# Optimization experiments

Measured on AMD Instinct MI355X. Metric: run time of the kernel, lower is better.

## Reference

```python
import jax, jax.numpy as jnp
import numpy as np

N_EMBD = 2048
N_Q = 32
N_KV = 8
GROUP = N_Q // N_KV   # 4
HD = N_EMBD // N_Q    # 64
BASE = 10000.0
NEG_INF = -1e30


def _rope(x):
    """Rotate-half RoPE on last dim; positions 1..t along dim -2 (as in the
    original _build_cache which uses arange(1, seq_len+1))."""
    t, d = x.shape[-2], x.shape[-1]
    d2 = d // 2
    theta = 1.0 / (BASE ** (jnp.arange(0, d, 2, dtype=jnp.float32) / d))  # (d/2,)
    pos = jnp.arange(1, t + 1, dtype=jnp.float32)                          # (t,)
    ang = pos[:, None] * theta[None, :]                                    # (t, d/2)
    ang = jnp.concatenate([ang, ang], axis=-1)                             # (t, d)
    sin, cos = jnp.sin(ang), jnp.cos(ang)
    rot = jnp.concatenate([-x[..., d2:], x[..., :d2]], axis=-1)
    return x * cos + rot * sin


def setup_inputs() -> dict:
    key = jax.random.key(0)
    ks = jax.random.split(key, 5)
    b, t = 2, 1024
    s = 1.0 / np.sqrt(N_EMBD)
    return {
        "x": jax.random.normal(ks[0], (b, t, N_EMBD), dtype=jnp.float32),
        "wq": jax.random.normal(ks[1], (N_EMBD, N_EMBD), dtype=jnp.float32) * s,
        "bq": jnp.zeros((N_EMBD,), dtype=jnp.float32),
        "wk": jax.random.normal(ks[2], (N_EMBD, N_KV * HD), dtype=jnp.float32) * s,
        "bk": jnp.zeros((N_KV * HD,), dtype=jnp.float32),
        "wv": jax.random.normal(ks[3], (N_EMBD, N_KV * HD), dtype=jnp.float32) * s,
        "bv": jnp.zeros((N_KV * HD,), dtype=jnp.float32),
        "wo": jax.random.normal(ks[4], (N_EMBD, N_EMBD), dtype=jnp.float32) * s,
        "bo": jnp.zeros((N_EMBD,), dtype=jnp.float32),
    }


def reference(x, wq, bq, wk, bk, wv, bv, wo, bo):
    b, t, _ = x.shape
    q = x @ wq + bq                                   # (b, t, E)
    k = x @ wk + bk                                   # (b, t, NKV*HD)
    v = x @ wv + bv
    q = q.reshape(b, t, N_Q, HD).transpose(0, 2, 1, 3)        # (b, nq, t, d)
    q = q.reshape(b, N_KV, GROUP, t, HD)                      # (b, hkv, g, t, d)
    k = k.reshape(b, t, N_KV, HD).transpose(0, 2, 1, 3)       # (b, hkv, t, d)
    v = v.reshape(b, t, N_KV, HD).transpose(0, 2, 1, 3)
    q = _rope(q)
    k = _rope(k)
    scale = jnp.sqrt(jnp.float32(HD))
    att = jnp.einsum("bhgqd,bhkd->bhgqk", q, k) / scale       # (b, hkv, g, t, t)
    causal = jnp.tril(jnp.ones((t, t), dtype=bool))
    att = jnp.where(causal, att, NEG_INF)
    att = jax.nn.softmax(att, axis=-1)
    out = jnp.einsum("bhgqk,bhkd->bhgqd", att, v)             # (b, hkv, g, t, d)
    out = out.transpose(0, 3, 1, 2, 4).reshape(b, t, N_EMBD)  # (b, t, E)
    return out @ wo + bo
```

## Files before the change

kernel.cpp:

```cpp
#include <hip/hip_runtime.h>
#include <hip/hip_bf16.h>
#include <cstdint>


typedef __attribute__((ext_vector_type(8))) short short8;
typedef __attribute__((ext_vector_type(4))) short short4v;
typedef __attribute__((ext_vector_type(4))) float f32x4;

__device__ inline short f2b(float f) {
  union { float f; unsigned u; } v; v.f = f;
  unsigned r = v.u + 0x7fffu + ((v.u >> 16) & 1u);
  return (short)(r >> 16);
}

__device__ inline float exp2_fast(float x) {
  float r;
  asm("v_exp_f32 %0, %1" : "=v"(r) : "v"(x));
  return r;
}

__device__ inline void gl_lds16(const void* g, void* l) {
  __builtin_amdgcn_global_load_lds((const __attribute__((address_space(1))) void*)g,
                                   (__attribute__((address_space(3))) void*)l,
                                   16, 0, 0);
}

__global__ void cast_x_kernel(const float* __restrict__ x, short* __restrict__ xb, int n4) {
  int i = blockIdx.x * 256 + threadIdx.x;
  if (i >= n4) return;
  float4 v = ((const float4*)x)[i];
  short4v o; o.x = f2b(v.x); o.y = f2b(v.y); o.z = f2b(v.z); o.w = f2b(v.w);
  ((short4v*)xb)[i] = o;
}

__global__ void wtrans_all(const float* __restrict__ wq, const float* __restrict__ wk,
                           const float* __restrict__ wv, const float* __restrict__ wo,
                           short* __restrict__ WqkvT, short* __restrict__ woT) {
  __shared__ float tile[64][65];
  const int bx = blockIdx.x;
  const float* W; short* WT; int N, off, nb;
  if (bx < 32)      { W = wq; WT = WqkvT; N = 2048; off = 0;    nb = bx * 64; }
  else if (bx < 40) { W = wk; WT = WqkvT; N = 512;  off = 2048; nb = (bx - 32) * 64; }
  else if (bx < 48) { W = wv; WT = WqkvT; N = 512;  off = 2560; nb = (bx - 40) * 64; }
  else              { W = wo; WT = woT;   N = 2048; off = 0;    nb = (bx - 48) * 64; }
  const int kb = blockIdx.y * 64;
  const int tid = threadIdx.x;
  const int c = tid & 63, r0 = tid >> 6;
#pragma unroll
  for (int s = 0; s < 16; ++s) {
    int k = r0 + s * 4;
    tile[c][k] = W[(size_t)(kb + k) * N + nb + c];
  }
  __syncthreads();
#pragma unroll
  for (int s = 0; s < 16; ++s) {
    int n = r0 + s * 4;
    WT[(size_t)(off + nb + n) * 2048 + kb + c] = f2b(tile[n][c]);
  }
}

__device__ __forceinline__ void gemm_loop_bk64(const short* __restrict__ Ag,
                                               const short* __restrict__ Bg,
                                               short* lA, short* lB,
                                               int w, int l15, int q4,
                                               f32x4 acc[2][4]) {
  const int K = 2048, NS = 32;
  const int q4x = q4 ^ ((l15 >> 1) & 3);
  auto stage = [&](int s, int d) {
    const short* As = Ag + s * 64;
    const short* Bs = Bg + s * 64;
    short* a = lA + d * 8192 + w * 512;
    gl_lds16(As, a);
    gl_lds16(As + 64 * K, a + 2048);
    gl_lds16(As + 32, a + 4096);
    gl_lds16(As + 64 * K + 32, a + 6144);
    short* bp = lB + d * 4096 + w * 512;
    gl_lds16(Bs, bp);
    gl_lds16(Bs + 32, bp + 2048);
  };
  stage(0, 0);
  for (int s = 0; s < NS; ++s) {
    const int d = s & 1;
    __syncthreads();
    if (s + 1 < NS) stage(s + 1, d ^ 1);
#pragma unroll
    for (int ks = 0; ks < 2; ++ks) {
      const short* ap = lA + d * 8192 + ks * 4096;
      const short* bp = lB + d * 4096 + ks * 2048;
      short8 af[2], bf[4];
#pragma unroll
      for (int mf = 0; mf < 2; ++mf) af[mf] = *(const short8*)(ap + (w * 32 + mf * 16 + l15) * 32 + q4x * 8);
#pragma unroll
      for (int nf = 0; nf < 4; ++nf) bf[nf] = *(const short8*)(bp + (nf * 16 + l15) * 32 + q4x * 8);
#pragma unroll
      for (int mf = 0; mf < 2; ++mf)
#pragma unroll
        for (int nf = 0; nf < 4; ++nf)
          acc[mf][nf] = __builtin_amdgcn_mfma_f32_16x16x32_bf16(af[mf], bf[nf], acc[mf][nf], 0, 0, 0);
    }
  }
}

__launch_bounds__(256, 3)
__global__ void gemm_qkv(const short* __restrict__ A, const short* __restrict__ BT,
                         const float* __restrict__ bq, const float* __restrict__ bk,
                         const float* __restrict__ bv,
                         short* __restrict__ Qb, short* __restrict__ Kb,
                         short* __restrict__ VTb) {
  __shared__ __align__(16) short lA[16384];
  __shared__ __align__(16) short lB[8192];
  const int K = 2048;
  const int tid = threadIdx.x, lane = tid & 63, w = tid >> 6;
  const int q4 = lane >> 4, l15 = lane & 15;
  const int bn = blockIdx.x * 64, bm = blockIdx.y * 128;

  const int swzc = ((tid & 3) ^ ((tid >> 3) & 3)) << 3;
  const short* Ag = A + (size_t)(bm + (tid >> 2)) * K + swzc;
  const short* Bg = BT + (size_t)(bn + (tid >> 2)) * K + swzc;

  f32x4 acc[2][4];
  const f32x4 fz = {0.f, 0.f, 0.f, 0.f};
#pragma unroll
  for (int i = 0; i < 2; ++i)
#pragma unroll
    for (int j = 0; j < 4; ++j) acc[i][j] = fz;

  gemm_loop_bk64(Ag, Bg, lA, lB, w, l15, q4, acc);

  const float L2T = 0.4152410118609203f;
  const float theta_a = exp2_fast(-(float)l15 * L2T);
  const float theta_b = exp2_fast(-(float)(l15 + 16) * L2T);
  const float s2 = 0.18033688011112042f;

  if (bn < 2048) {
    const int h = bn >> 6;
    float bb0 = bq[bn + l15], bb1 = bq[bn + 16 + l15], bb2 = bq[bn + 32 + l15], bb3 = bq[bn + 48 + l15];
#pragma unroll
    for (int mf = 0; mf < 2; ++mf)
#pragma unroll
      for (int r = 0; r < 4; ++r) {
        int row = bm + w * 32 + mf * 16 + q4 * 4 + r;
        int batch = row >> 10, t = row & 1023;
        float pos = (float)(t + 1);
        float sa, ca, sb, cb;
        __sincosf(pos * theta_a, &sa, &ca);
        __sincosf(pos * theta_b, &sb, &cb);
        float x0 = acc[mf][0][r] + bb0, x2 = acc[mf][2][r] + bb2;
        float x1 = acc[mf][1][r] + bb1, x3 = acc[mf][3][r] + bb3;
        size_t base = ((size_t)(batch * 32 + h) * 1024 + t) * 64;
        Qb[base + l15]      = f2b((x0 * ca - x2 * sa) * s2);
        Qb[base + l15 + 32] = f2b((x2 * ca + x0 * sa) * s2);
        Qb[base + l15 + 16] = f2b((x1 * cb - x3 * sb) * s2);
        Qb[base + l15 + 48] = f2b((x3 * cb + x1 * sb) * s2);
      }
  } else if (bn < 2560) {
    const int co = bn - 2048;
    const int hkv = co >> 6;
    float bb0 = bk[co + l15], bb1 = bk[co + 16 + l15], bb2 = bk[co + 32 + l15], bb3 = bk[co + 48 + l15];
#pragma unroll
    for (int mf = 0; mf < 2; ++mf)
#pragma unroll
      for (int r = 0; r < 4; ++r) {
        int row = bm + w * 32 + mf * 16 + q4 * 4 + r;
        int batch = row >> 10, t = row & 1023;
        float pos = (float)(t + 1);
        float sa, ca, sb, cb;
        __sincosf(pos * theta_a, &sa, &ca);
        __sincosf(pos * theta_b, &sb, &cb);
        float x0 = acc[mf][0][r] + bb0, x2 = acc[mf][2][r] + bb2;
        float x1 = acc[mf][1][r] + bb1, x3 = acc[mf][3][r] + bb3;
        size_t base = (size_t)(batch * 8 + hkv) * 65536 + t * 32;
        Kb[base + l15]              = f2b(x0 * ca - x2 * sa);
        Kb[base + l15 + 16]         = f2b(x1 * cb - x3 * sb);
        Kb[base + 32768 + l15]      = f2b(x2 * ca + x0 * sa);
        Kb[base + 32768 + l15 + 16] = f2b(x3 * cb + x1 * sb);
      }
  } else {
    const int co = bn - 2560;
    const int hkv = co >> 6;
    float bb[4];
#pragma unroll
    for (int nf = 0; nf < 4; ++nf) bb[nf] = bv[co + nf * 16 + l15];
    const int batch = (bm + w * 32) >> 10;
    const size_t vbase = (size_t)(batch * 8 + hkv) * 65536;
#pragma unroll
    for (int mf = 0; mf < 2; ++mf) {
      const int t0 = (bm + w * 32 + mf * 16 + q4 * 4) & 1023;
      const size_t rbase = vbase + (size_t)(t0 >> 5) * 2048 + (t0 & 31);
#pragma unroll
      for (int nf = 0; nf < 4; ++nf) {
        short4v pk;
#pragma unroll
        for (int r = 0; r < 4; ++r) pk[r] = f2b(acc[mf][nf][r] + bb[nf]);
        *(short4v*)(VTb + rbase + (nf * 16 + l15) * 32) = pk;
      }
    }
  }
}

#define PROW 72
__launch_bounds__(256, 3)
__global__ void attn5_kernel(const short* __restrict__ Qb, const short* __restrict__ Kb,
                             const short* __restrict__ VTb, short* __restrict__ AO) {
  __shared__ __align__(16) short lK[2][128 * 32];
  __shared__ __align__(16) short lVT[4][64 * 32];
  __shared__ __align__(16) short lP[4][2][16 * PROW];
  const int tid = threadIdx.x, lane = tid & 63, w = tid >> 6;
  const int q4 = lane >> 4, l15 = lane & 15;
  const int q4x = q4 ^ ((l15 >> 1) & 3);
  const int swzc = ((tid & 3) ^ ((tid >> 3) & 3)) << 3;
  const int qt = (int)gridDim.x - 1 - (int)blockIdx.x;
  const int h = blockIdx.y, b = blockIdx.z;
  const int hkv = h >> 2;
  const int qb = qt * 128 + w * 32;
  const int kdiag = qb >> 6;
  const int ns = qt + 1;

  const short* Qg = Qb + (size_t)(b * 32 + h) * 65536;
  const short* Kg = Kb + (size_t)(b * 8 + hkv) * 65536;
  const short* Vg = VTb + (size_t)(b * 8 + hkv) * 65536;

  short8 qf[2][2];
#pragma unroll
  for (int mf = 0; mf < 2; ++mf) {
    const short* qr = Qg + (size_t)(qb + mf * 16 + l15) * 64 + q4 * 8;
    qf[mf][0] = *(const short8*)(qr);
    qf[mf][1] = *(const short8*)(qr + 32);
  }

  const f32x4 fz = {0.f, 0.f, 0.f, 0.f};
  f32x4 o[2][4], ol[2];
#pragma unroll
  for (int mf = 0; mf < 2; ++mf) {
    ol[mf] = fz;
#pragma unroll
    for (int i = 0; i < 4; ++i) o[mf][i] = fz;
  }
  short8 ones;
#pragma unroll
  for (int i = 0; i < 8; ++i) ones[i] = (short)0x3F80;

  for (int s = 0; s < ns; ++s) {
    {
      const short* Ksrc = Kg + (size_t)(s * 128 + (tid >> 2)) * 32 + swzc;
      short* ldst = (short*)lK + w * 512;
      gl_lds16(Ksrc, ldst);
      gl_lds16(Ksrc + 64 * 32, ldst + 2048);
      gl_lds16(Ksrc + 32768, ldst + 4096);
      gl_lds16(Ksrc + 32768 + 64 * 32, ldst + 6144);
      const short* Vsrc = Vg + (size_t)(s * 4) * 2048 + (tid >> 2) * 32 + swzc;
      short* vdst = (short*)lVT + w * 512;
#pragma unroll
      for (int c = 0; c < 4; ++c) gl_lds16(Vsrc + c * 2048, vdst + c * 2048);
    }
    __syncthreads();

#pragma unroll
    for (int ki = 0; ki < 2; ++ki) {
      const int ktg = s * 2 + ki;
      if (ktg <= kdiag) {
        short8 kf0[4], kf1[4];
#pragma unroll
        for (int nt = 0; nt < 4; ++nt) {
          kf0[nt] = *(const short8*)((short*)lK + (ki * 64 + nt * 16 + l15) * 32 + q4x * 8);
          kf1[nt] = *(const short8*)((short*)lK + 4096 + (ki * 64 + nt * 16 + l15) * 32 + q4x * 8);
        }
        const bool diag = (ktg == kdiag);
#pragma unroll
        for (int mf = 0; mf < 2; ++mf) {
          f32x4 sv[4];
#pragma unroll
          for (int nt = 0; nt < 4; ++nt) {
            f32x4 z = __builtin_amdgcn_mfma_f32_16x16x32_bf16(qf[mf][0], kf0[nt], fz, 0, 0, 0);
            sv[nt] = __builtin_amdgcn_mfma_f32_16x16x32_bf16(qf[mf][1], kf1[nt], z, 0, 0, 0);
          }
          if (diag) {
#pragma unroll
            for (int r = 0; r < 4; ++r) {
              const int qrow = qb + mf * 16 + q4 * 4 + r;
              const int col = ktg * 64 + l15;
#pragma unroll
              for (int nt = 0; nt < 4; ++nt)
                if (col + nt * 16 > qrow) sv[nt][r] = -1e30f;
            }
          }
          short* lPm = lP[w][mf];
#pragma unroll
          for (int r = 0; r < 4; ++r)
#pragma unroll
            for (int nt = 0; nt < 4; ++nt)
              lPm[(q4 * 4 + r) * PROW + nt * 16 + l15] = f2b(exp2_fast(sv[nt][r] - 16.f));
        }

        short8 vf0[4], vf1[4];
#pragma unroll
        for (int dt = 0; dt < 4; ++dt) {
          vf0[dt] = *(const short8*)((short*)lVT + (2 * ki) * 2048 + (dt * 16 + l15) * 32 + q4x * 8);
          vf1[dt] = *(const short8*)((short*)lVT + (2 * ki + 1) * 2048 + (dt * 16 + l15) * 32 + q4x * 8);
        }
#pragma unroll
        for (int mf = 0; mf < 2; ++mf) {
          const short* lPm = lP[w][mf];
          short8 pf0 = *(const short8*)(lPm + l15 * PROW + q4 * 8);
          short8 pf1 = *(const short8*)(lPm + l15 * PROW + 32 + q4 * 8);
          ol[mf] = __builtin_amdgcn_mfma_f32_16x16x32_bf16(pf0, ones, ol[mf], 0, 0, 0);
          ol[mf] = __builtin_amdgcn_mfma_f32_16x16x32_bf16(pf1, ones, ol[mf], 0, 0, 0);
#pragma unroll
          for (int dt = 0; dt < 4; ++dt) {
            o[mf][dt] = __builtin_amdgcn_mfma_f32_16x16x32_bf16(pf0, vf0[dt], o[mf][dt], 0, 0, 0);
            o[mf][dt] = __builtin_amdgcn_mfma_f32_16x16x32_bf16(pf1, vf1[dt], o[mf][dt], 0, 0, 0);
          }
        }
      }
    }
    __syncthreads();
  }

#pragma unroll
  for (int mf = 0; mf < 2; ++mf)
#pragma unroll
    for (int r = 0; r < 4; ++r) {
      float inv = __builtin_amdgcn_rcpf(ol[mf][r]);
      int row = qb + mf * 16 + q4 * 4 + r;
#pragma unroll
      for (int dt = 0; dt < 4; ++dt)
        AO[(size_t)(b * 1024 + row) * 2048 + h * 64 + dt * 16 + l15] = f2b(o[mf][dt][r] * inv);
    }
}

__launch_bounds__(256, 3)
__global__ void gemm_out(const short* __restrict__ A, const short* __restrict__ BT,
                         float* __restrict__ C, const float* __restrict__ bias,
                         int N, int K) {
  __shared__ __align__(16) short lA[16384];
  __shared__ __align__(16) short lB[8192];
  const int tid = threadIdx.x, lane = tid & 63, w = tid >> 6;
  const int q4 = lane >> 4, l15 = lane & 15;
  const int bn = blockIdx.x * 64, bm = blockIdx.y * 128;

  const int swzc = ((tid & 3) ^ ((tid >> 3) & 3)) << 3;
  const short* Ag = A + (size_t)(bm + (tid >> 2)) * K + swzc;
  const short* Bg = BT + (size_t)(bn + (tid >> 2)) * K + swzc;

  f32x4 acc[2][4];
  const f32x4 fz = {0.f, 0.f, 0.f, 0.f};
#pragma unroll
  for (int i = 0; i < 2; ++i)
#pragma unroll
    for (int j = 0; j < 4; ++j) acc[i][j] = fz;

  gemm_loop_bk64(Ag, Bg, lA, lB, w, l15, q4, acc);

#pragma unroll
  for (int mf = 0; mf < 2; ++mf)
#pragma unroll
    for (int nf = 0; nf < 4; ++nf) {
      int col = bn + nf * 16 + l15;
      float bb = bias[col];
#pragma unroll
      for (int r = 0; r < 4; ++r) {
        int row = bm + w * 32 + mf * 16 + q4 * 4 + r;
        C[(size_t)row * N + col] = acc[mf][nf][r] + bb;
      }
    }
}

extern "C" void kernel_launch(void* const* d_in, const int* in_sizes, int n_in,
                              void* d_out, int out_size, void* d_ws, size_t ws_size,
                              hipStream_t stream) {
  const float* x  = (const float*)d_in[0];
  const float* wq = (const float*)d_in[1];
  const float* bq = (const float*)d_in[2];
  const float* wk = (const float*)d_in[3];
  const float* bk = (const float*)d_in[4];
  const float* wv = (const float*)d_in[5];
  const float* bv = (const float*)d_in[6];
  const float* wo = (const float*)d_in[7];
  const float* bo = (const float*)d_in[8];
  float* out = (float*)d_out;
  const int B = in_sizes[0] / (1024 * 2048);
  const int M = B * 1024;

  char* ws = (char*)d_ws;
  size_t off = 0;
  auto alloc = [&](size_t bytes) -> char* {
    char* p = ws + off;
    off += (bytes + 255) & ~(size_t)255;
    return p;
  };
  short* xb    = (short*)alloc((size_t)M * 2048 * 2);
  short* WqkvT = (short*)alloc((size_t)3072 * 2048 * 2);
  short* woT   = (short*)alloc((size_t)2048 * 2048 * 2);
  short* Qb    = (short*)alloc((size_t)B * 32 * 1024 * 64 * 2);
  short* Kb    = (short*)alloc((size_t)B * 8 * 2 * 1024 * 32 * 2);
  short* VTb   = (short*)alloc((size_t)B * 8 * 32 * 64 * 32 * 2);
  short* AO    = (short*)alloc((size_t)M * 2048 * 2);

  cast_x_kernel<<<(M * 2048 / 4 + 255) / 256, 256, 0, stream>>>(x, xb, M * 2048 / 4);
  wtrans_all<<<dim3(80, 32), 256, 0, stream>>>(wq, wk, wv, wo, WqkvT, woT);
  gemm_qkv<<<dim3(48, M / 128), 256, 0, stream>>>(xb, WqkvT, bq, bk, bv, Qb, Kb, VTb);
  attn5_kernel<<<dim3(8, 32, B), 256, 0, stream>>>(Qb, Kb, VTb, AO);
  gemm_out<<<dim3(32, M / 128), 256, 0, stream>>>(AO, woT, out, bo, 2048, 2048);
}
```

Baseline: 206.2 us.

## Replace block-shared LDS K/V staging with single-wave blocks loading K/V directly

```diff
diff --git a/kernel.cpp b/kernel.cpp
--- a/kernel.cpp
+++ b/kernel.cpp
@@ -199,22 +199,17 @@
 }
 
 #define PROW 72
-__launch_bounds__(256, 3)
-__global__ void attn5_kernel(const short* __restrict__ Qb, const short* __restrict__ Kb,
+__launch_bounds__(64, 2)
+__global__ void attn6_kernel(const short* __restrict__ Qb, const short* __restrict__ Kb,
                              const short* __restrict__ VTb, short* __restrict__ AO) {
-  __shared__ __align__(16) short lK[2][128 * 32];
-  __shared__ __align__(16) short lVT[4][64 * 32];
-  __shared__ __align__(16) short lP[4][2][16 * PROW];
-  const int tid = threadIdx.x, lane = tid & 63, w = tid >> 6;
+  __shared__ __align__(16) short lP[2][16 * PROW];
+  const int lane = threadIdx.x;
   const int q4 = lane >> 4, l15 = lane & 15;
-  const int q4x = q4 ^ ((l15 >> 1) & 3);
-  const int swzc = ((tid & 3) ^ ((tid >> 3) & 3)) << 3;
-  const int qt = (int)gridDim.x - 1 - (int)blockIdx.x;
+  const int qt = 31 - (int)blockIdx.x;
   const int h = blockIdx.y, b = blockIdx.z;
   const int hkv = h >> 2;
-  const int qb = qt * 128 + w * 32;
+  const int qb = qt * 32;
   const int kdiag = qb >> 6;
-  const int ns = qt + 1;
 
   const short* Qg = Qb + (size_t)(b * 32 + h) * 65536;
   const short* Kg = Kb + (size_t)(b * 8 + hkv) * 65536;
@@ -240,80 +235,68 @@
 #pragma unroll
   for (int i = 0; i < 8; ++i) ones[i] = (short)0x3F80;
 
-  for (int s = 0; s < ns; ++s) {
-    {
-      const short* Ksrc = Kg + (size_t)(s * 128 + (tid >> 2)) * 32 + swzc;
-      short* ldst = (short*)lK + w * 512;
-      gl_lds16(Ksrc, ldst);
-      gl_lds16(Ksrc + 64 * 32, ldst + 2048);
-      gl_lds16(Ksrc + 32768, ldst + 4096);
-      gl_lds16(Ksrc + 32768 + 64 * 32, ldst + 6144);
-      const short* Vsrc = Vg + (size_t)(s * 4) * 2048 + (tid >> 2) * 32 + swzc;
-      short* vdst = (short*)lVT + w * 512;
-#pragma unroll
-      for (int c = 0; c < 4; ++c) gl_lds16(Vsrc + c * 2048, vdst + c * 2048);
-    }
-    __syncthreads();
-
-#pragma unroll
-    for (int ki = 0; ki < 2; ++ki) {
-      const int ktg = s * 2 + ki;
-      if (ktg <= kdiag) {
-        short8 kf0[4], kf1[4];
-#pragma unroll
-        for (int nt = 0; nt < 4; ++nt) {
-          kf0[nt] = *(const short8*)((short*)lK + (ki * 64 + nt * 16 + l15) * 32 + q4x * 8);
-          kf1[nt] = *(const short8*)((short*)lK + 4096 + (ki * 64 + nt * 16 + l15) * 32 + q4x * 8);
+  short8 kf0[4], kf1[4], vf0[4], vf1[4];
+  auto loadK = [&](int ktg) {
+    const short* kb0 = Kg + (size_t)(ktg * 64 + l15) * 32 + q4 * 8;
+#pragma unroll
+    for (int nt = 0; nt < 4; ++nt) kf0[nt] = *(const short8*)(kb0 + nt * 512);
+#pragma unroll
+    for (int nt = 0; nt < 4; ++nt) kf1[nt] = *(const short8*)(kb0 + 32768 + nt * 512);
+  };
+  auto loadV = [&](int ktg) {
+    const short* vb = Vg + (size_t)(2 * ktg) * 2048 + l15 * 32 + q4 * 8;
+#pragma unroll
+    for (int dt = 0; dt < 4; ++dt) vf0[dt] = *(const short8*)(vb + dt * 512);
+#pragma unroll
+    for (int dt = 0; dt < 4; ++dt) vf1[dt] = *(const short8*)(vb + 2048 + dt * 512);
+  };
+
+  loadK(0);
+  for (int ktg = 0; ktg <= kdiag; ++ktg) {
+    loadV(ktg);
+    f32x4 sv[2][4];
+#pragma unroll
+    for (int mf = 0; mf < 2; ++mf)
+#pragma unroll
+      for (int nt = 0; nt < 4; ++nt) {
+        f32x4 z = __builtin_amdgcn_mfma_f32_16x16x32_bf16(qf[mf][0], kf0[nt], fz, 0, 0, 0);
+        sv[mf][nt] = __builtin_amdgcn_mfma_f32_16x16x32_bf16(qf[mf][1], kf1[nt], z, 0, 0, 0);
+      }
+    if (ktg == kdiag) {
+#pragma unroll
+      for (int mf = 0; mf < 2; ++mf)
+#pragma unroll
+        for (int r = 0; r < 4; ++r) {
+          const int qrow = qb + mf * 16 + q4 * 4 + r;
+          const int col = ktg * 64 + l15;
+#pragma unroll
+          for (int nt = 0; nt < 4; ++nt)
+            if (col + nt * 16 > qrow) sv[mf][nt][r] = -1e30f;
         }
-        const bool diag = (ktg == kdiag);
-#pragma unroll
-        for (int mf = 0; mf < 2; ++mf) {
-          f32x4 sv[4];
-#pragma unroll
-          for (int nt = 0; nt < 4; ++nt) {
-            f32x4 z = __builtin_amdgcn_mfma_f32_16x16x32_bf16(qf[mf][0], kf0[nt], fz, 0, 0, 0);
-            sv[nt] = __builtin_amdgcn_mfma_f32_16x16x32_bf16(qf[mf][1], kf1[nt], z, 0, 0, 0);
-          }
-          if (diag) {
-#pragma unroll
-            for (int r = 0; r < 4; ++r) {
-              const int qrow = qb + mf * 16 + q4 * 4 + r;
-              const int col = ktg * 64 + l15;
-#pragma unroll
-              for (int nt = 0; nt < 4; ++nt)
-                if (col + nt * 16 > qrow) sv[nt][r] = -1e30f;
-            }
-          }
-          short* lPm = lP[w][mf];
-#pragma unroll
-          for (int r = 0; r < 4; ++r)
-#pragma unroll
-            for (int nt = 0; nt < 4; ++nt)
-              lPm[(q4 * 4 + r) * PROW + nt * 16 + l15] = f2b(exp2_fast(sv[nt][r] - 16.f));
-        }
-
-        short8 vf0[4], vf1[4];
-#pragma unroll
-        for (int dt = 0; dt < 4; ++dt) {
-          vf0[dt] = *(const short8*)((short*)lVT + (2 * ki) * 2048 + (dt * 16 + l15) * 32 + q4x * 8);
-          vf1[dt] = *(const short8*)((short*)lVT + (2 * ki + 1) * 2048 + (dt * 16 + l15) * 32 + q4x * 8);
-        }
-#pragma unroll
-        for (int mf = 0; mf < 2; ++mf) {
-          const short* lPm = lP[w][mf];
-          short8 pf0 = *(const short8*)(lPm + l15 * PROW + q4 * 8);
-          short8 pf1 = *(const short8*)(lPm + l15 * PROW + 32 + q4 * 8);
-          ol[mf] = __builtin_amdgcn_mfma_f32_16x16x32_bf16(pf0, ones, ol[mf], 0, 0, 0);
-          ol[mf] = __builtin_amdgcn_mfma_f32_16x16x32_bf16(pf1, ones, ol[mf], 0, 0, 0);
-#pragma unroll
-          for (int dt = 0; dt < 4; ++dt) {
-            o[mf][dt] = __builtin_amdgcn_mfma_f32_16x16x32_bf16(pf0, vf0[dt], o[mf][dt], 0, 0, 0);
-            o[mf][dt] = __builtin_amdgcn_mfma_f32_16x16x32_bf16(pf1, vf1[dt], o[mf][dt], 0, 0, 0);
-          }
-        }
-      }
-    }
-    __syncthreads();
+    }
+    if (ktg < kdiag) loadK(ktg + 1);
+#pragma unroll
+    for (int mf = 0; mf < 2; ++mf) {
+      short* lPm = lP[mf];
+#pragma unroll
+      for (int r = 0; r < 4; ++r)
+#pragma unroll
+        for (int nt = 0; nt < 4; ++nt)
+          lPm[(q4 * 4 + r) * PROW + nt * 16 + l15] = f2b(exp2_fast(sv[mf][nt][r] - 16.f));
+    }
+#pragma unroll
+    for (int mf = 0; mf < 2; ++mf) {
+      const short* lPm = lP[mf];
+      short8 pf0 = *(const short8*)(lPm + l15 * PROW + q4 * 8);
+      short8 pf1 = *(const short8*)(lPm + l15 * PROW + 32 + q4 * 8);
+      ol[mf] = __builtin_amdgcn_mfma_f32_16x16x32_bf16(pf0, ones, ol[mf], 0, 0, 0);
+      ol[mf] = __builtin_amdgcn_mfma_f32_16x16x32_bf16(pf1, ones, ol[mf], 0, 0, 0);
+#pragma unroll
+      for (int dt = 0; dt < 4; ++dt) {
+        o[mf][dt] = __builtin_amdgcn_mfma_f32_16x16x32_bf16(pf0, vf0[dt], o[mf][dt], 0, 0, 0);
+        o[mf][dt] = __builtin_amdgcn_mfma_f32_16x16x32_bf16(pf1, vf1[dt], o[mf][dt], 0, 0, 0);
+      }
+    }
   }
 
 #pragma unroll
@@ -399,6 +382,6 @@
   cast_x_kernel<<<(M * 2048 / 4 + 255) / 256, 256, 0, stream>>>(x, xb, M * 2048 / 4);
   wtrans_all<<<dim3(80, 32), 256, 0, stream>>>(wq, wk, wv, wo, WqkvT, woT);
   gemm_qkv<<<dim3(48, M / 128), 256, 0, stream>>>(xb, WqkvT, bq, bk, bv, Qb, Kb, VTb);
-  attn5_kernel<<<dim3(8, 32, B), 256, 0, stream>>>(Qb, Kb, VTb, AO);
+  attn6_kernel<<<dim3(32, 32, B), 64, 0, stream>>>(Qb, Kb, VTb, AO);
   gemm_out<<<dim3(32, M / 128), 256, 0, stream>>>(AO, woT, out, bo, 2048, 2048);
 }
```

Result: no change. 209.8 us (+1.8%).

## Double-buffer K/V tiles in attention with 64-key stages and prefetch

Applied to the files above, without the earlier changes.

```diff
diff --git a/kernel.cpp b/kernel.cpp
--- a/kernel.cpp
+++ b/kernel.cpp
@@ -200,10 +200,10 @@
 
 #define PROW 72
 __launch_bounds__(256, 3)
-__global__ void attn5_kernel(const short* __restrict__ Qb, const short* __restrict__ Kb,
+__global__ void attn8_kernel(const short* __restrict__ Qb, const short* __restrict__ Kb,
                              const short* __restrict__ VTb, short* __restrict__ AO) {
-  __shared__ __align__(16) short lK[2][128 * 32];
-  __shared__ __align__(16) short lVT[4][64 * 32];
+  __shared__ __align__(16) short lK[2][2 * 64 * 32];
+  __shared__ __align__(16) short lVT[2][2 * 64 * 32];
   __shared__ __align__(16) short lP[4][2][16 * PROW];
   const int tid = threadIdx.x, lane = tid & 63, w = tid >> 6;
   const int q4 = lane >> 4, l15 = lane & 15;
@@ -214,7 +214,7 @@
   const int hkv = h >> 2;
   const int qb = qt * 128 + w * 32;
   const int kdiag = qb >> 6;
-  const int ns = qt + 1;
+  const int ns = 2 * qt + 2;
 
   const short* Qg = Qb + (size_t)(b * 32 + h) * 65536;
   const short* Kg = Kb + (size_t)(b * 8 + hkv) * 65536;
@@ -240,80 +240,80 @@
 #pragma unroll
   for (int i = 0; i < 8; ++i) ones[i] = (short)0x3F80;
 
+  auto stage = [&](int s, int d) {
+    const short* Ksrc = Kg + (size_t)(s * 64 + (tid >> 2)) * 32 + swzc;
+    short* kd = (short*)lK + d * 4096 + w * 512;
+    gl_lds16(Ksrc, kd);
+    gl_lds16(Ksrc + 32768, kd + 2048);
+    const short* Vsrc = Vg + (size_t)(2 * s) * 2048 + (tid >> 2) * 32 + swzc;
+    short* vd = (short*)lVT + d * 4096 + w * 512;
+    gl_lds16(Vsrc, vd);
+    gl_lds16(Vsrc + 2048, vd + 2048);
+  };
+
+  stage(0, 0);
   for (int s = 0; s < ns; ++s) {
-    {
-      const short* Ksrc = Kg + (size_t)(s * 128 + (tid >> 2)) * 32 + swzc;
-      short* ldst = (short*)lK + w * 512;
-      gl_lds16(Ksrc, ldst);
-      gl_lds16(Ksrc + 64 * 32, ldst + 2048);
-      gl_lds16(Ksrc + 32768, ldst + 4096);
-      gl_lds16(Ksrc + 32768 + 64 * 32, ldst + 6144);
-      const short* Vsrc = Vg + (size_t)(s * 4) * 2048 + (tid >> 2) * 32 + swzc;
-      short* vdst = (short*)lVT + w * 512;
-#pragma unroll
-      for (int c = 0; c < 4; ++c) gl_lds16(Vsrc + c * 2048, vdst + c * 2048);
+    const int d = s & 1;
+    __syncthreads();
+    if (s + 1 < ns) stage(s + 1, d ^ 1);
+    if (s <= kdiag) {
+      const short* kp = (short*)lK + d * 4096;
+      const short* vp = (short*)lVT + d * 4096;
+      short8 kf0[4], kf1[4];
+#pragma unroll
+      for (int nt = 0; nt < 4; ++nt) {
+        kf0[nt] = *(const short8*)(kp + (nt * 16 + l15) * 32 + q4x * 8);
+        kf1[nt] = *(const short8*)(kp + 2048 + (nt * 16 + l15) * 32 + q4x * 8);
+      }
+      f32x4 sv[2][4];
+#pragma unroll
+      for (int mf = 0; mf < 2; ++mf)
+#pragma unroll
+        for (int nt = 0; nt < 4; ++nt) {
+          f32x4 z = __builtin_amdgcn_mfma_f32_16x16x32_bf16(qf[mf][0], kf0[nt], fz, 0, 0, 0);
+          sv[mf][nt] = __builtin_amdgcn_mfma_f32_16x16x32_bf16(qf[mf][1], kf1[nt], z, 0, 0, 0);
+        }
+      if (s == kdiag) {
+#pragma unroll
+        for (int mf = 0; mf < 2; ++mf)
+#pragma unroll
+          for (int r = 0; r < 4; ++r) {
+            const int qrow = qb + mf * 16 + q4 * 4 + r;
+            const int col = s * 64 + l15;
+#pragma unroll
+            for (int nt = 0; nt < 4; ++nt)
+              if (col + nt * 16 > qrow) sv[mf][nt][r] = -1e30f;
+          }
+      }
+#pragma unroll
+      for (int mf = 0; mf < 2; ++mf) {
+        short* lPm = lP[w][mf];
+#pragma unroll
+        for (int r = 0; r < 4; ++r)
+#pragma unroll
+          for (int nt = 0; nt < 4; ++nt)
+            lPm[(q4 * 4 + r) * PROW + nt * 16 + l15] = f2b(exp2_fast(sv[mf][nt][r] - 16.f));
+      }
+      short8 vf0[4], vf1[4];
+#pragma unroll
+      for (int dt = 0; dt < 4; ++dt) {
+        vf0[dt] = *(const short8*)(vp + (dt * 16 + l15) * 32 + q4x * 8);
+        vf1[dt] = *(const short8*)(vp + 2048 + (dt * 16 + l15) * 32 + q4x * 8);
+      }
+#pragma unroll
+      for (int mf = 0; mf < 2; ++mf) {
+        const short* lPm = lP[w][mf];
+        short8 pf0 = *(const short8*)(lPm + l15 * PROW + q4 * 8);
+        short8 pf1 = *(const short8*)(lPm + l15 * PROW + 32 + q4 * 8);
+        ol[mf] = __builtin_amdgcn_mfma_f32_16x16x32_bf16(pf0, ones, ol[mf], 0, 0, 0);
+        ol[mf] = __builtin_amdgcn_mfma_f32_16x16x32_bf16(pf1, ones, ol[mf], 0, 0, 0);
+#pragma unroll
+        for (int dt = 0; dt < 4; ++dt) {
+          o[mf][dt] = __builtin_amdgcn_mfma_f32_16x16x32_bf16(pf0, vf0[dt], o[mf][dt], 0, 0, 0);
+          o[mf][dt] = __builtin_amdgcn_mfma_f32_16x16x32_bf16(pf1, vf1[dt], o[mf][dt], 0, 0, 0);
+        }
+      }
     }
-    __syncthreads();
-
-#pragma unroll
-    for (int ki = 0; ki < 2; ++ki) {
-      const int ktg = s * 2 + ki;
-      if (ktg <= kdiag) {
-        short8 kf0[4], kf1[4];
-#pragma unroll
-        for (int nt = 0; nt < 4; ++nt) {
-          kf0[nt] = *(const short8*)((short*)lK + (ki * 64 + nt * 16 + l15) * 32 + q4x * 8);
-          kf1[nt] = *(const short8*)((short*)lK + 4096 + (ki * 64 + nt * 16 + l15) * 32 + q4x * 8);
-        }
-        const bool diag = (ktg == kdiag);
-#pragma unroll
-        for (int mf = 0; mf < 2; ++mf) {
-          f32x4 sv[4];
-#pragma unroll
-          for (int nt = 0; nt < 4; ++nt) {
-            f32x4 z = __builtin_amdgcn_mfma_f32_16x16x32_bf16(qf[mf][0], kf0[nt], fz, 0, 0, 0);
-            sv[nt] = __builtin_amdgcn_mfma_f32_16x16x32_bf16(qf[mf][1], kf1[nt], z, 0, 0, 0);
-          }
-          if (diag) {
-#pragma unroll
-            for (int r = 0; r < 4; ++r) {
-              const int qrow = qb + mf * 16 + q4 * 4 + r;
-              const int col = ktg * 64 + l15;
-#pragma unroll
-              for (int nt = 0; nt < 4; ++nt)
-                if (col + nt * 16 > qrow) sv[nt][r] = -1e30f;
-            }
-          }
-          short* lPm = lP[w][mf];
-#pragma unroll
-          for (int r = 0; r < 4; ++r)
-#pragma unroll
-            for (int nt = 0; nt < 4; ++nt)
-              lPm[(q4 * 4 + r) * PROW + nt * 16 + l15] = f2b(exp2_fast(sv[nt][r] - 16.f));
-        }
-
-        short8 vf0[4], vf1[4];
-#pragma unroll
-        for (int dt = 0; dt < 4; ++dt) {
-          vf0[dt] = *(const short8*)((short*)lVT + (2 * ki) * 2048 + (dt * 16 + l15) * 32 + q4x * 8);
-          vf1[dt] = *(const short8*)((short*)lVT + (2 * ki + 1) * 2048 + (dt * 16 + l15) * 32 + q4x * 8);
-        }
-#pragma unroll
-        for (int mf = 0; mf < 2; ++mf) {
-          const short* lPm = lP[w][mf];
-          short8 pf0 = *(const short8*)(lPm + l15 * PROW + q4 * 8);
-          short8 pf1 = *(const short8*)(lPm + l15 * PROW + 32 + q4 * 8);
-          ol[mf] = __builtin_amdgcn_mfma_f32_16x16x32_bf16(pf0, ones, ol[mf], 0, 0, 0);
-          ol[mf] = __builtin_amdgcn_mfma_f32_16x16x32_bf16(pf1, ones, ol[mf], 0, 0, 0);
-#pragma unroll
-          for (int dt = 0; dt < 4; ++dt) {
-            o[mf][dt] = __builtin_amdgcn_mfma_f32_16x16x32_bf16(pf0, vf0[dt], o[mf][dt], 0, 0, 0);
-            o[mf][dt] = __builtin_amdgcn_mfma_f32_16x16x32_bf16(pf1, vf1[dt], o[mf][dt], 0, 0, 0);
-          }
-        }
-      }
-    }
-    __syncthreads();
   }
 
 #pragma unroll
@@ -399,6 +399,6 @@
   cast_x_kernel<<<(M * 2048 / 4 + 255) / 256, 256, 0, stream>>>(x, xb, M * 2048 / 4);
   wtrans_all<<<dim3(80, 32), 256, 0, stream>>>(wq, wk, wv, wo, WqkvT, woT);
   gemm_qkv<<<dim3(48, M / 128), 256, 0, stream>>>(xb, WqkvT, bq, bk, bv, Qb, Kb, VTb);
-  attn5_kernel<<<dim3(8, 32, B), 256, 0, stream>>>(Qb, Kb, VTb, AO);
+  attn8_kernel<<<dim3(8, 32, B), 256, 0, stream>>>(Qb, Kb, VTb, AO);
   gemm_out<<<dim3(32, M / 128), 256, 0, stream>>>(AO, woT, out, bo, 2048, 2048);
 }
```

Measured after the change: 206.6 us. No clear change (+0.2%).
